# Kernel optimization log

Measured on AMD Instinct MI355X. Metric: run time of the kernel, lower is better.

Reference implementation:

```python
import math
import jax, jax.numpy as jnp
import numpy as np
from jax import lax

B = 8
IN_CH = 512
OUT_CH = 256
K = 3
LATENT = 512
BLUR = [1, 3, 3, 1]
FACTOR = 2
H = W = 64
# p = len(blur) - factor - (K-1) = 0 -> pad = ((p+1)//2 + factor - 1, p//2 + 1) = (1, 1)
PAD0, PAD1 = 1, 1


def _make_blur_kernel():
    k = jnp.array(BLUR, jnp.float32)
    k = k[None, :] * k[:, None]          # separable -> 2D
    k = k / jnp.sum(k)
    return k * (FACTOR ** 2)             # make_kernel(blur, factor) scales by factor^2


def setup_inputs() -> dict:
    key = jax.random.key(0)
    k1, k2, k3, k4 = jax.random.split(key, 4)
    inputs = {
        "input": jax.random.normal(k1, (B, IN_CH, H, W), jnp.float32),
        "w": jax.random.normal(k2, (B, LATENT), jnp.float32),
        # learned params
        "affine_weight": jax.random.normal(k3, (IN_CH, LATENT), jnp.float32),
        "affine_bias": jnp.ones((IN_CH,), jnp.float32),  # bias_init=1
        "conv_weight": jax.random.normal(k4, (1, OUT_CH, IN_CH, K, K), jnp.float32),
    }
    return inputs


def reference(input, w, affine_weight, affine_bias, conv_weight):
    batch = input.shape[0]
    # EqualLinear: scale = 1/sqrt(latent_dim), lr_mul=1
    style = w @ (affine_weight * (1.0 / math.sqrt(LATENT))).T + affine_bias  # (B, IN_CH)
    # modulate
    scale = 1.0 / math.sqrt(IN_CH * K * K)
    weight = (scale * conv_weight) * style[:, None, :, None, None]          # (B, OUT, IN, K, K)
    # demodulate over (in, kh, kw)
    demod = lax.rsqrt(jnp.sum(weight * weight, axis=(2, 3, 4)) + 1e-8)      # (B, OUT)
    weight = weight * demod[:, :, None, None, None]
    # grouped conv_transpose2d (groups=batch, stride=2, pad=0) == per-sample
    # conv with lhs_dilation=2, spatial padding K-1, kernel spatially flipped.
    kflip = jnp.flip(weight, (-2, -1))                                      # (B, OUT, IN, K, K) OIHW

    def ct(x, kern):  # x: (IN, H, W), kern: (OUT, IN, K, K)
        return lax.conv_general_dilated(
            x[None], kern, window_strides=(1, 1),
            padding=[(K - 1, K - 1), (K - 1, K - 1)],
            lhs_dilation=(2, 2),
            dimension_numbers=("NCHW", "OIHW", "NCHW"))[0]

    out = jax.vmap(ct)(input, kflip)                                        # (B, OUT, 2H-2+K, 2W-2+K)
    # upfirdn2d with up=down=1: pad then depthwise correlate with flipped FIR kernel
    blur = jnp.flip(_make_blur_kernel())                                    # (4, 4)
    out = jnp.pad(out, ((0, 0), (0, 0), (PAD0, PAD1), (PAD0, PAD1)))
    dw = jnp.tile(blur[None, None], (OUT_CH, 1, 1, 1))                      # (OUT, 1, 4, 4)
    out = lax.conv_general_dilated(
        out, dw, window_strides=(1, 1), padding="VALID",
        feature_group_count=OUT_CH,
        dimension_numbers=("NCHW", "OIHW", "NCHW"))
    return out  # (B, OUT, 2H, 2W)
```

## Files before the change

kernel.cpp:

```cpp
#include <hip/hip_runtime.h>
#include <hip/hip_bf16.h>
#include <math.h>

#define NB 8
#define INCH 512
#define OUTCH 256
#define SP 4096
#define LAT 512
#define NTAP 9
#define MDIM (NTAP*OUTCH)

#define INV_SQRT_LAT 0.044194173824159216f
#define WSCALE 0.014731391274719738f

typedef __bf16 bf16x8 __attribute__((ext_vector_type(8)));
typedef float  f32x4  __attribute__((ext_vector_type(4)));

__device__ __forceinline__ unsigned short f2bf(float f) {
  unsigned u = __float_as_uint(f);
  u += 0x7fffu + ((u >> 16) & 1u);
  return (unsigned short)(u >> 16);
}
__device__ __forceinline__ float bf2f(unsigned short v) {
  return __uint_as_float((unsigned)v << 16);
}

__global__ void style_k(const float* __restrict__ w, const float* __restrict__ aff,
                        const float* __restrict__ bias, float* __restrict__ style) {
  int gid = blockIdx.x * 256 + threadIdx.x;
  int b = gid >> 9, i = gid & 511;
  const float4* wv = (const float4*)(w + (size_t)b * LAT);
  const float4* av = (const float4*)(aff + (size_t)i * LAT);
  float s = 0.f;
#pragma unroll 4
  for (int l = 0; l < LAT / 4; ++l) {
    float4 a = av[l], ww = wv[l];
    s += a.x * ww.x + a.y * ww.y + a.z * ww.z + a.w * ww.w;
  }
  style[gid] = s * INV_SQRT_LAT + bias[i];
}

__global__ void wprep_k(const float* __restrict__ cw, float* __restrict__ S,
                        unsigned short* __restrict__ w9) {
  int gid = blockIdx.x * 256 + threadIdx.x;
  int o = gid >> 9, i = gid & 511;
  const float* p = cw + (size_t)gid * 9;
  float ss = 0.f, v[9];
#pragma unroll
  for (int t = 0; t < 9; ++t) { v[t] = p[t]; ss += v[t] * v[t]; }
  S[gid] = ss * (WSCALE * WSCALE);
#pragma unroll
  for (int t = 0; t < 9; ++t)
    w9[((size_t)(t * OUTCH + o)) * INCH + i] = f2bf(v[t] * WSCALE);
}

__global__ void demod_k(const float* __restrict__ style, const float* __restrict__ S,
                        float* __restrict__ dmod) {
  int gid = blockIdx.x * 256 + threadIdx.x;
  int b = gid >> 8, o = gid & 255;
  const float4* sv = (const float4*)(style + (size_t)b * INCH);
  const float4* Sv = (const float4*)(S + (size_t)o * INCH);
  float acc = 0.f;
#pragma unroll 4
  for (int l = 0; l < INCH / 4; ++l) {
    float4 st = sv[l], s2 = Sv[l];
    acc += st.x * st.x * s2.x + st.y * st.y * s2.y + st.z * st.z * s2.z + st.w * st.w * s2.w;
  }
  dmod[gid] = 1.0f / sqrtf(acc + 1e-8f);
}

__global__ void modx_k(const float* __restrict__ x, const float* __restrict__ style,
                       unsigned short* __restrict__ xmt) {
  __shared__ float tile[32][33];
  int b = blockIdx.z;
  int s0 = blockIdx.x * 32;
  int i0 = blockIdx.y * 32;
  int c = threadIdx.x & 31, r = threadIdx.x >> 5;
#pragma unroll
  for (int p = 0; p < 4; ++p) {
    int ii = r + p * 8;
    tile[ii][c] = x[((size_t)(b * INCH + i0 + ii)) * SP + s0 + c] * style[b * INCH + i0 + ii];
  }
  __syncthreads();
#pragma unroll
  for (int p = 0; p < 4; ++p) {
    int ss = r + p * 8;
    xmt[((size_t)(b * SP + s0 + ss)) * INCH + i0 + c] = f2bf(tile[c][ss]);
  }
}

__global__ __launch_bounds__(256, 2)
void gemm_k(const unsigned short* __restrict__ A,
            const unsigned short* __restrict__ Bm,
            unsigned short* __restrict__ C) {
  __shared__ __align__(16) unsigned short As[128 * 64];
  __shared__ __align__(16) unsigned short Bs[128 * 64];
  Bm += (size_t)blockIdx.z * SP * INCH;
  C  += (size_t)blockIdx.z * MDIM * SP;
  const int tid  = threadIdx.x;
  const int lane = tid & 63;
  const int wave = tid >> 6;
  const int m0 = blockIdx.y * 128;
  const int n0 = blockIdx.x * 128;
  const int wm = (wave >> 1) * 64;
  const int wn = (wave & 1) * 64;
  const int lrow   = lane >> 3;
  const int gchunk = (lane & 7) ^ lrow;

  f32x4 acc[4][4];
#pragma unroll
  for (int i = 0; i < 4; ++i)
#pragma unroll
    for (int j = 0; j < 4; ++j) acc[i][j] = (f32x4){0.f, 0.f, 0.f, 0.f};

  const int r16  = lane & 15;
  const int quad = lane >> 4;

  for (int k0 = 0; k0 < INCH; k0 += 64) {
#pragma unroll
    for (int it = 0; it < 4; ++it) {
      int rbase = it * 32 + wave * 8;
      const unsigned short* ga = A  + (size_t)(m0 + rbase + lrow) * INCH + k0 + gchunk * 8;
      const unsigned short* gb = Bm + (size_t)(n0 + rbase + lrow) * INCH + k0 + gchunk * 8;
      __builtin_amdgcn_global_load_lds((const __attribute__((address_space(1))) void*)ga,
                                       (__attribute__((address_space(3))) void*)&As[rbase * 64],
                                       16, 0, 0);
      __builtin_amdgcn_global_load_lds((const __attribute__((address_space(1))) void*)gb,
                                       (__attribute__((address_space(3))) void*)&Bs[rbase * 64],
                                       16, 0, 0);
    }
    __syncthreads();
#pragma unroll
    for (int kk = 0; kk < 2; ++kk) {
      bf16x8 af[4], bfr[4];
#pragma unroll
      for (int i = 0; i < 4; ++i) {
        int rowa = wm + i * 16 + r16;
        int cha  = (kk * 4 + quad) ^ (rowa & 7);
        af[i] = *(const bf16x8*)&As[rowa * 64 + cha * 8];
        int rowb = wn + i * 16 + r16;
        int chb  = (kk * 4 + quad) ^ (rowb & 7);
        bfr[i] = *(const bf16x8*)&Bs[rowb * 64 + chb * 8];
      }
#pragma unroll
      for (int i = 0; i < 4; ++i)
#pragma unroll
        for (int j = 0; j < 4; ++j)
          acc[i][j] = __builtin_amdgcn_mfma_f32_16x16x32_bf16(af[i], bfr[j], acc[i][j], 0, 0, 0);
    }
    __syncthreads();
  }
#pragma unroll
  for (int i = 0; i < 4; ++i)
#pragma unroll
    for (int j = 0; j < 4; ++j)
#pragma unroll
      for (int r = 0; r < 4; ++r) {
        int mrow = m0 + wm + i * 16 + quad * 4 + r;
        int ncol = n0 + wn + j * 16 + r16;
        C[(size_t)mrow * SP + ncol] = f2bf(acc[i][j][r]);
      }
}

#define TLS 342
#define VS  648
__global__ void combine_k(const unsigned short* __restrict__ T, const float* __restrict__ dm,
                          float* __restrict__ out) {
  __shared__ __align__(16) float Tl[9 * TLS];
  __shared__ __align__(16) float V[3 * VS];
  T   += (size_t)blockIdx.z * MDIM * SP;
  dm  += (size_t)blockIdx.z * OUTCH;
  out += (size_t)blockIdx.z * OUTCH * 128 * 128;
  const int o = blockIdx.y;
  const int Ty = blockIdx.x >> 2, Tx = blockIdx.x & 3;
  const int tid = threadIdx.x;
  for (int idx = tid; idx < 9 * 324; idx += 256) {
    int tap = idx / 324;
    int rem = idx - tap * 324;
    int yy = rem / 18;
    int xx = rem - yy * 18;
    int Yg = Ty * 16 - 1 + yy;
    int Xg = Tx * 16 - 1 + xx;
    float v = 0.f;
    if ((unsigned)Yg < 64u && (unsigned)Xg < 64u)
      v = bf2f(T[((size_t)(tap * OUTCH + o)) * SP + Yg * 64 + Xg]);
    Tl[tap * TLS + yy * 19 + xx] = v;
  }
  __syncthreads();
  {
    int r = tid >> 2;
    if (r < 54) {
      int c = r / 18;
      int yr = r - c * 18;
      int X0 = (tid & 3) * 4;
      const float* base = &Tl[c * 3 * TLS + yr * 19 + X0];
      float t0[6], t1[6], t2[6];
#pragma unroll
      for (int k = 0; k < 6; ++k) {
        t0[k] = base[k];
        t1[k] = base[TLS + k];
        t2[k] = base[2 * TLS + k];
      }
      float* vrow = &V[c * VS + yr * 36 + X0 * 2];
#pragma unroll
      for (int Xl = 0; Xl < 4; ++Xl) {
        vrow[2 * Xl]     = t1[Xl] + 3.f * t2[Xl] + 3.f * t0[Xl + 1] + 3.f * t1[Xl + 1] + t2[Xl + 1] + t0[Xl + 2];
        vrow[2 * Xl + 1] = t2[Xl] + t0[Xl + 1] + 3.f * t1[Xl + 1] + 3.f * t2[Xl + 1] + 3.f * t0[Xl + 2] + t1[Xl + 2];
      }
    }
  }
  __syncthreads();
  const int y  = tid >> 3;
  const int py = y & 1;
  const int Yl = y >> 1;
  const int xp0 = (tid & 7) * 4;
  f32x4 vv[3][3];
#pragma unroll
  for (int c = 0; c < 3; ++c)
#pragma unroll
    for (int jj = 0; jj < 3; ++jj)
      vv[c][jj] = *(const f32x4*)&V[c * VS + (Yl + jj) * 36 + xp0];
  f32x4 o4;
  if (py == 0)
    o4 = vv[1][0] + 3.f * vv[2][0] + 3.f * vv[0][1] + 3.f * vv[1][1] + vv[2][1] + vv[0][2];
  else
    o4 = vv[2][0] + vv[0][1] + 3.f * vv[1][1] + 3.f * vv[2][1] + 3.f * vv[0][2] + vv[1][2];
  float dmv = dm[o] * (1.0f / 16.0f);
  o4 *= dmv;
  *(f32x4*)&out[((size_t)o * 128 + Ty * 32 + y) * 128 + Tx * 32 + xp0] = o4;
}

extern "C" void kernel_launch(void* const* d_in, const int* in_sizes, int n_in,
                              void* d_out, int out_size, void* d_ws, size_t ws_size,
                              hipStream_t stream) {
  const float* x    = (const float*)d_in[0];
  const float* w    = (const float*)d_in[1];
  const float* aff  = (const float*)d_in[2];
  const float* bias = (const float*)d_in[3];
  const float* cw   = (const float*)d_in[4];
  float* out = (float*)d_out;
  char* ws = (char*)d_ws;
  float* style        = (float*)(ws);
  float* S            = (float*)(ws + 16384);
  float* dmod         = (float*)(ws + 540672);
  unsigned short* w9  = (unsigned short*)(ws + 548864);
  unsigned short* xmt = (unsigned short*)(ws + 2908160);
  unsigned short* T   = (unsigned short*)(ws + 36462592);

  hipLaunchKernelGGL(style_k, dim3(16), dim3(256), 0, stream, w, aff, bias, style);
  hipLaunchKernelGGL(wprep_k, dim3(512), dim3(256), 0, stream, cw, S, w9);
  hipLaunchKernelGGL(demod_k, dim3(8), dim3(256), 0, stream, style, S, dmod);
  hipLaunchKernelGGL(modx_k, dim3(128, 16, 8), dim3(256), 0, stream, x, style, xmt);
  hipLaunchKernelGGL(gemm_k, dim3(32, 18, NB), dim3(256), 0, stream, w9, xmt, T);
  hipLaunchKernelGGL(combine_k, dim3(16, 256, NB), dim3(256), 0, stream, T, dmod, out);
}
```

Baseline: 439.8 us.

## Stage GEMM epilogue through LDS for coalesced stores and widen combine tiles

The GEMM epilogue now writes the bf16 accumulators into a shared staging buffer, one half-block of waves at a time, then emits 16-byte coalesced row stores instead of scattered 2-byte writes. The combine kernel now handles full 64-wide rows per block (16 input rows), loads T with vectorized reads, keeps the tile in LDS as bf16 and produces 32 outputs per thread in the horizontal pass. The aim is to cut uncoalesced global traffic and halo overhead in both kernels. The cost is extra LDS use and barriers in the GEMM, which may lower occupancy, plus higher register pressure in combine.

```diff
diff --git a/kernel.cpp b/kernel.cpp
--- a/kernel.cpp
+++ b/kernel.cpp
@@ -95,6 +95,7 @@
             unsigned short* __restrict__ C) {
   __shared__ __align__(16) unsigned short As[128 * 64];
   __shared__ __align__(16) unsigned short Bs[128 * 64];
+  __shared__ __align__(16) unsigned short stage[64 * 136];
   Bm += (size_t)blockIdx.z * SP * INCH;
   C  += (size_t)blockIdx.z * MDIM * SP;
   const int tid  = threadIdx.x;
@@ -151,83 +152,145 @@
     __syncthreads();
   }
 #pragma unroll
-  for (int i = 0; i < 4; ++i)
-#pragma unroll
-    for (int j = 0; j < 4; ++j)
-#pragma unroll
-      for (int r = 0; r < 4; ++r) {
-        int mrow = m0 + wm + i * 16 + quad * 4 + r;
-        int ncol = n0 + wn + j * 16 + r16;
-        C[(size_t)mrow * SP + ncol] = f2bf(acc[i][j][r]);
-      }
-}
-
-#define TLS 342
-#define VS  648
-__global__ void combine_k(const unsigned short* __restrict__ T, const float* __restrict__ dm,
-                          float* __restrict__ out) {
-  __shared__ __align__(16) float Tl[9 * TLS];
-  __shared__ __align__(16) float V[3 * VS];
+  for (int p = 0; p < 2; ++p) {
+    if ((wave >> 1) == p) {
+#pragma unroll
+      for (int i = 0; i < 4; ++i) {
+        int mr = i * 16 + quad * 4;
+#pragma unroll
+        for (int j = 0; j < 4; ++j) {
+          int ncb = ((wn + j * 16 + r16) + quad * 8) & 127;
+#pragma unroll
+          for (int r = 0; r < 4; ++r)
+            stage[(mr + r) * 136 + ncb] = f2bf(acc[i][j][r]);
+        }
+      }
+    }
+    __syncthreads();
+    {
+      int lr = tid >> 2;
+      int qr = (lr >> 2) & 3;
+      int quarter = tid & 3;
+      const unsigned short* srow = stage + lr * 136;
+      size_t gbase = (size_t)(m0 + p * 64 + lr) * SP + n0 + quarter * 32;
+#pragma unroll
+      for (int k = 0; k < 4; ++k) {
+        int lchunk = quarter * 4 + k;
+        int pchunk = (lchunk + qr) & 15;
+        uint4 val = *(const uint4*)(srow + pchunk * 8);
+        *(uint4*)(&C[gbase + k * 8]) = val;
+      }
+    }
+    __syncthreads();
+  }
+}
+
+#define TLSTR 78
+#define VSTR  136
+__global__ __launch_bounds__(256)
+void combine_k(const unsigned short* __restrict__ T, const float* __restrict__ dm,
+               float* __restrict__ out) {
+  __shared__ __align__(16) unsigned short TlB[9 * 18 * TLSTR + 8];
+  __shared__ __align__(16) float V[3 * 18 * VSTR];
   T   += (size_t)blockIdx.z * MDIM * SP;
   dm  += (size_t)blockIdx.z * OUTCH;
   out += (size_t)blockIdx.z * OUTCH * 128 * 128;
-  const int o = blockIdx.y;
-  const int Ty = blockIdx.x >> 2, Tx = blockIdx.x & 3;
+  const int o  = blockIdx.y;
+  const int Y0 = blockIdx.x * 16;
   const int tid = threadIdx.x;
-  for (int idx = tid; idx < 9 * 324; idx += 256) {
-    int tap = idx / 324;
-    int rem = idx - tap * 324;
-    int yy = rem / 18;
-    int xx = rem - yy * 18;
-    int Yg = Ty * 16 - 1 + yy;
-    int Xg = Tx * 16 - 1 + xx;
-    float v = 0.f;
-    if ((unsigned)Yg < 64u && (unsigned)Xg < 64u)
-      v = bf2f(T[((size_t)(tap * OUTCH + o)) * SP + Yg * 64 + Xg]);
-    Tl[tap * TLS + yy * 19 + xx] = v;
+
+  {
+    uint4* tz = (uint4*)TlB;
+#pragma unroll
+    for (int idx = tid; idx < 1580; idx += 256) tz[idx] = (uint4){0u, 0u, 0u, 0u};
   }
   __syncthreads();
+
   {
-    int r = tid >> 2;
+    const int c16 = tid & 15;
+    const int r0  = tid >> 4;
+#pragma unroll
+    for (int tap = 0; tap < 9; ++tap) {
+      const unsigned short* tp = T + (size_t)(tap * OUTCH + o) * SP;
+#pragma unroll
+      for (int rr = 0; rr < 2; ++rr) {
+        int ry = r0 + rr * 16;
+        if (ry < 18) {
+          int Yg = Y0 - 1 + ry;
+          if ((unsigned)Yg < 64u) {
+            ushort4 v4 = *(const ushort4*)(tp + Yg * 64 + c16 * 4);
+            unsigned short* dst = &TlB[(tap * 18 + ry) * TLSTR + 4 + c16 * 4];
+            *(ushort2*)(dst)     = make_ushort2(v4.x, v4.y);
+            *(ushort2*)(dst + 2) = make_ushort2(v4.z, v4.w);
+          }
+        }
+      }
+    }
+  }
+  __syncthreads();
+
+  {
+    const int r = tid >> 2;
     if (r < 54) {
-      int c = r / 18;
-      int yr = r - c * 18;
-      int X0 = (tid & 3) * 4;
-      const float* base = &Tl[c * 3 * TLS + yr * 19 + X0];
-      float t0[6], t1[6], t2[6];
-#pragma unroll
-      for (int k = 0; k < 6; ++k) {
-        t0[k] = base[k];
-        t1[k] = base[TLS + k];
-        t2[k] = base[2 * TLS + k];
-      }
-      float* vrow = &V[c * VS + yr * 36 + X0 * 2];
-#pragma unroll
-      for (int Xl = 0; Xl < 4; ++Xl) {
-        vrow[2 * Xl]     = t1[Xl] + 3.f * t2[Xl] + 3.f * t0[Xl + 1] + 3.f * t1[Xl + 1] + t2[Xl + 1] + t0[Xl + 2];
-        vrow[2 * Xl + 1] = t2[Xl] + t0[Xl + 1] + 3.f * t1[Xl + 1] + 3.f * t2[Xl + 1] + 3.f * t0[Xl + 2] + t1[Xl + 2];
-      }
+      const int c  = r / 18;
+      const int yr = r - c * 18;
+      const int X0 = (tid & 3) * 16;
+      float td[3][20];
+#pragma unroll
+      for (int d = 0; d < 3; ++d) {
+        const unsigned short* src = &TlB[((c * 3 + d) * 18 + yr) * TLSTR + 2 + X0];
+#pragma unroll
+        for (int k = 0; k < 10; ++k) {
+          ushort2 u2 = *(const ushort2*)(src + 2 * k);
+          td[d][2 * k]     = bf2f(u2.x);
+          td[d][2 * k + 1] = bf2f(u2.y);
+        }
+      }
+      float vout[32];
+#pragma unroll
+      for (int Xl = 0; Xl < 16; ++Xl) {
+        float a0 = td[0][Xl + 1], a1 = td[0][Xl + 2], a2 = td[0][Xl + 3];
+        float b0 = td[1][Xl + 1], b1 = td[1][Xl + 2], b2 = td[1][Xl + 3];
+        float c0 = td[2][Xl + 1], c1 = td[2][Xl + 2], c2 = td[2][Xl + 3];
+        vout[2 * Xl]     = b0 + 3.f * c0 + 3.f * a1 + 3.f * b1 + c1 + a2;
+        vout[2 * Xl + 1] = c0 + a1 + 3.f * b1 + 3.f * c1 + 3.f * a2 + b2;
+      }
+      float* vr = &V[(c * 18 + yr) * VSTR + 2 * X0];
+#pragma unroll
+      for (int q = 0; q < 8; ++q)
+        *(f32x4*)(vr + 4 * q) = (f32x4){vout[4 * q], vout[4 * q + 1], vout[4 * q + 2], vout[4 * q + 3]};
     }
   }
   __syncthreads();
-  const int y  = tid >> 3;
-  const int py = y & 1;
-  const int Yl = y >> 1;
-  const int xp0 = (tid & 7) * 4;
-  f32x4 vv[3][3];
-#pragma unroll
-  for (int c = 0; c < 3; ++c)
-#pragma unroll
-    for (int jj = 0; jj < 3; ++jj)
-      vv[c][jj] = *(const f32x4*)&V[c * VS + (Yl + jj) * 36 + xp0];
-  f32x4 o4;
-  if (py == 0)
-    o4 = vv[1][0] + 3.f * vv[2][0] + 3.f * vv[0][1] + 3.f * vv[1][1] + vv[2][1] + vv[0][2];
-  else
-    o4 = vv[2][0] + vv[0][1] + 3.f * vv[1][1] + 3.f * vv[2][1] + 3.f * vv[0][2] + vv[1][2];
-  float dmv = dm[o] * (1.0f / 16.0f);
-  o4 *= dmv;
-  *(f32x4*)&out[((size_t)o * 128 + Ty * 32 + y) * 128 + Tx * 32 + xp0] = o4;
+
+  {
+    const int y  = tid >> 3;
+    const int py = y & 1;
+    const int Yl = y >> 1;
+    const int xq = (tid & 7) * 4;
+    const float dmv = dm[o] * (1.0f / 16.0f);
+    float* orow = out + ((size_t)o * 128 + (Y0 * 2 + y)) * 128;
+#pragma unroll
+    for (int xg = 0; xg < 4; ++xg) {
+      int xp = xq + xg * 32;
+      f32x4 v00 = *(const f32x4*)&V[(0 * 18 + Yl + 0) * VSTR + xp];
+      f32x4 v01 = *(const f32x4*)&V[(0 * 18 + Yl + 1) * VSTR + xp];
+      f32x4 v02 = *(const f32x4*)&V[(0 * 18 + Yl + 2) * VSTR + xp];
+      f32x4 v10 = *(const f32x4*)&V[(1 * 18 + Yl + 0) * VSTR + xp];
+      f32x4 v11 = *(const f32x4*)&V[(1 * 18 + Yl + 1) * VSTR + xp];
+      f32x4 v12 = *(const f32x4*)&V[(1 * 18 + Yl + 2) * VSTR + xp];
+      f32x4 v20 = *(const f32x4*)&V[(2 * 18 + Yl + 0) * VSTR + xp];
+      f32x4 v21 = *(const f32x4*)&V[(2 * 18 + Yl + 1) * VSTR + xp];
+      f32x4 v22 = *(const f32x4*)&V[(2 * 18 + Yl + 2) * VSTR + xp];
+      f32x4 r;
+      if (py == 0)
+        r = v10 + 3.f * v20 + 3.f * v01 + 3.f * v11 + v21 + v02;
+      else
+        r = v20 + v01 + 3.f * v11 + 3.f * v21 + 3.f * v02 + v12;
+      r *= dmv;
+      *(f32x4*)(orow + xp) = r;
+    }
+  }
 }
 
 extern "C" void kernel_launch(void* const* d_in, const int* in_sizes, int n_in,
@@ -252,5 +315,5 @@
   hipLaunchKernelGGL(demod_k, dim3(8), dim3(256), 0, stream, style, S, dmod);
   hipLaunchKernelGGL(modx_k, dim3(128, 16, 8), dim3(256), 0, stream, x, style, xmt);
   hipLaunchKernelGGL(gemm_k, dim3(32, 18, NB), dim3(256), 0, stream, w9, xmt, T);
-  hipLaunchKernelGGL(combine_k, dim3(16, 256, NB), dim3(256), 0, stream, T, dmod, out);
-}
+  hipLaunchKernelGGL(combine_k, dim3(4, 256, NB), dim3(256), 0, stream, T, dmod, out);
+}
```

New measurement: 470.9 us. 7.1% more time.
